# Performance work log

Measured on AMD Instinct MI355X. Metric: run time of the kernel, lower is better.

## Reference

```python
import jax, jax.numpy as jnp
import numpy as np

B, C, HH, WW = 2, 64, 56, 56
NH, IP, OP = 4, 32, 64  # num_heads, inter_plane, out_plane
EPS = 1e-5


def setup_inputs() -> dict:
    key = jax.random.key(0)
    ks = jax.random.split(key, 12)
    r = lambda k, sh, s: jax.random.normal(k, sh, jnp.float32) * s
    inp = {
        "x": r(ks[0], (B, C, HH, WW), 1.0),
        # 1x1 conv QKV projections: weight [out_ch, in_ch], kaiming-ish scale
        "wk": r(ks[1], (NH * IP, C), C ** -0.5), "bk": jnp.zeros((NH * IP,), jnp.float32),
        "wq": r(ks[2], (NH * IP, C), C ** -0.5), "bq": jnp.zeros((NH * IP,), jnp.float32),
        "wv": r(ks[3], (NH * IP, C), C ** -0.5), "bv": jnp.zeros((NH * IP,), jnp.float32),
        # GCN linears
        "w1": r(ks[4], (OP, IP), IP ** -0.5), "b1": jnp.zeros((OP,), jnp.float32),
        "g1": 1.0 + r(ks[5], (NH * OP,), 0.1), "be1": jnp.zeros((NH * OP,), jnp.float32),
        "rm1": jnp.zeros((NH * OP,), jnp.float32), "rv1": jnp.ones((NH * OP,), jnp.float32),
        "w2": r(ks[6], (OP, OP), OP ** -0.5), "b2": jnp.zeros((OP,), jnp.float32),
        "g2": 1.0 + r(ks[7], (NH * OP,), 0.1), "be2": jnp.zeros((NH * OP,), jnp.float32),
        "rm2": jnp.zeros((NH * OP,), jnp.float32), "rv2": jnp.ones((NH * OP,), jnp.float32),
        # final 1x1 projection
        "wf": r(ks[8], (OP, NH * OP), (NH * OP) ** -0.5), "bf": jnp.zeros((OP,), jnp.float32),
    }
    return inp


def _conv1x1(x, w, b):
    # x: [b,c,h,w], w: [o,c] -> [b,o,h,w]
    return jnp.einsum('bchw,oc->bohw', x, w) + b[None, :, None, None]


def _bn_relu(y, g, be, rm, rv, b, n):
    # y: [b,H,N,OP]; BatchNorm1d(H*OP) in eval mode over channel axis, then ReLU
    z = y.transpose(0, 1, 3, 2).reshape(b, NH * OP, n)  # [b, H*OP, N]
    z = (z - rm[None, :, None]) * (g / jnp.sqrt(rv + EPS))[None, :, None] + be[None, :, None]
    return jax.nn.relu(z.reshape(b, NH, OP, n).transpose(0, 1, 3, 2))  # [b,H,N,OP]


def reference(x, wk, bk, wq, bq, wv, bv, w1, b1, g1, be1, rm1, rv1,
              w2, b2, g2, be2, rm2, rv2, wf, bf):
    b, c, h, w = x.shape
    n = h * w
    node_k = _conv1x1(x, wk, bk).reshape(b, NH, IP, n).transpose(0, 1, 3, 2)  # [b,H,N,IP]
    node_q = _conv1x1(x, wq, bq).reshape(b, NH, IP, n)                        # [b,H,IP,N]
    node_v = _conv1x1(x, wv, bv).reshape(b, NH, IP, n).transpose(0, 1, 3, 2)  # [b,H,N,IP]
    adj = jnp.einsum('bhnd,bhdm->bhnm', node_k, node_q)  # [b,H,N,N]
    adj = jax.nn.softmax(adj, axis=2)  # NOTE: torch softmax(dim=2) -> normalize over rows axis
    av = jnp.einsum('bhnm,bhmd->bhnd', adj, node_v)      # [b,H,N,IP]
    avw = _bn_relu(av @ w1.T + b1, g1, be1, rm1, rv1, b, n)   # [b,H,N,OP]; dropout is identity (eval)
    av2 = jnp.einsum('bhnm,bhmd->bhnd', adj, avw)        # [b,H,N,OP]
    avw2 = _bn_relu(av2 @ w2.T + b2, g2, be2, rm2, rv2, b, n)  # [b,H,N,OP]
    y = avw2.transpose(0, 1, 3, 2).reshape(b, NH * OP, h, w)
    return _conv1x1(y, wf, bf)  # [b, OP, h, w]
```

## Files before the change

### kernel.cpp

```cpp
#include <hip/hip_runtime.h>
#include <hip/hip_bf16.h>

typedef __hip_bfloat16 bf16;
typedef __attribute__((ext_vector_type(8))) short bfrag;
typedef __attribute__((ext_vector_type(4))) short s16x4;
typedef __attribute__((ext_vector_type(4))) float f32x4;
typedef __attribute__((ext_vector_type(16))) float f32x16;

#define MFMA32(a,b,c) __builtin_amdgcn_mfma_f32_32x32x16_bf16((a),(b),(c),0,0,0)

__device__ __forceinline__ float b2f(bf16 x){ return __bfloat162float(x); }
__device__ __forceinline__ bf16 f2b(float x){ return __float2bfloat16(x); }
__device__ __forceinline__ float fexp2(float x){ return __builtin_amdgcn_exp2f(x); }
__device__ __forceinline__ float us2f(unsigned short u){ unsigned v = (unsigned)u << 16; return __uint_as_float(v); }

#define NN   3136
#define NBH  8
#define NCH  7
#define MCH  448
#define LDP  40
#define LDPA 72
#define LOG2E 1.44269504f

__global__ __launch_bounds__(256) void k_zero(float* __restrict__ p, int n4)
{
    int i = blockIdx.x * 256 + threadIdx.x;
    if (i < n4) reinterpret_cast<f32x4*>(p)[i] = (f32x4){0.f, 0.f, 0.f, 0.f};
}

__global__ __launch_bounds__(256) void k_proj(
    const float* __restrict__ x,
    const float* __restrict__ wk, const float* __restrict__ bk,
    const float* __restrict__ wq, const float* __restrict__ bq,
    const float* __restrict__ wv, const float* __restrict__ bv,
    bf16* __restrict__ kt, bf16* __restrict__ qt, bf16* __restrict__ vt)
{
    __shared__ __align__(16) bf16 xT[32 * 72];
    __shared__ __align__(16) bf16 wT[128 * 72];
    int tid = threadIdx.x, w = tid >> 6, lane = tid & 63;
    int l31 = lane & 31, lsel = lane >> 5;
    int n0 = blockIdx.x * 32;
    int p  = blockIdx.y;
    int b  = blockIdx.z;
    const float* wp = (p == 0) ? wk : ((p == 1) ? wq : wv);
    const float* bp = (p == 0) ? bk : ((p == 1) ? bq : bv);

    for (int i = tid; i < 2048; i += 256) {
        int c = i >> 5, j = i & 31;
        xT[j * 72 + c] = f2b(x[((size_t)b * 64 + c) * NN + n0 + j]);
    }
    for (int i = tid; i < 8192; i += 256) {
        int oc = i >> 6, c = i & 63;
        wT[oc * 72 + c] = f2b(wp[oc * 64 + c]);
    }
    __syncthreads();

    f32x16 s;
    #pragma unroll
    for (int r = 0; r < 16; ++r) s[r] = 0.f;
    #pragma unroll
    for (int k = 0; k < 4; ++k) {
        bfrag a  = *(const bfrag*)(&xT[l31 * 72 + k * 16 + lsel * 8]);
        bfrag bw = *(const bfrag*)(&wT[(w * 32 + l31) * 72 + k * 16 + lsel * 8]);
        s = MFMA32(a, bw, s);
    }
    float bias = bp[w * 32 + l31];
    size_t bh = (size_t)b * 4 + w;
    if (p == 2) {
        #pragma unroll
        for (int q = 0; q < 4; ++q) {
            s16x4 pk;
            #pragma unroll
            for (int i = 0; i < 4; ++i) {
                bf16 e = f2b(s[4 * q + i] + bias);
                pk[i] = *(short*)&e;
            }
            *(s16x4*)(vt + (bh * 32 + l31) * NN + n0 + 8 * q + 4 * lsel) = pk;
        }
    } else {
        bf16* dst = (p == 0) ? kt : qt;
        float sc = (p == 0) ? LOG2E : 1.0f;
        #pragma unroll
        for (int r = 0; r < 16; ++r) {
            int nl = (r & 3) + 8 * (r >> 2) + 4 * lsel;
            dst[(bh * NN + n0 + nl) * 32 + l31] = f2b((s[r] + bias) * sc);
        }
    }
}

__global__ __launch_bounds__(256) void k_stats(const bf16* __restrict__ kt,
                                               const bf16* __restrict__ qt,
                                               float* __restrict__ den)
{
    __shared__ __align__(16) bf16 Kb[2][64 * LDP];
    int tid = threadIdx.x, w = tid >> 6, lane = tid & 63;
    int l31 = lane & 31, lsel = lane >> 5;
    int bh = blockIdx.z;
    int mt = blockIdx.x * 4 + w;
    bool act = (mt < 98);
    int m0 = (act ? mt : 97) * 32;
    int ns = blockIdx.y * MCH;

    const bf16* qp = qt + ((size_t)bh * NN + m0 + l31) * 32 + lsel * 8;
    bfrag qb0 = *(const bfrag*)qp;
    bfrag qb1 = *(const bfrag*)(qp + 16);
    const bf16* kt_bh = kt + (size_t)bh * NN * 32;

    int sr = tid >> 2, sc = (tid & 3) * 8;
    const bf16* sbase = kt_bh + (size_t)(ns + sr) * 32 + sc;
    int soff = sr * LDP + sc;

    *(bfrag*)(&Kb[0][soff]) = *(const bfrag*)sbase;
    __syncthreads();

    float dacc = 0.f;
    for (int t = 0; t < 7; ++t) {
        bfrag pre;
        bool hn = (t + 1 < 7);
        if (hn) pre = *(const bfrag*)(sbase + (size_t)(t + 1) * 2048);
        const bf16* kl = &Kb[t & 1][0];
        #pragma unroll
        for (int nt = 0; nt < 2; ++nt) {
            int ko = (l31 + 32 * nt) * LDP + lsel * 8;
            bfrag kb0 = *(const bfrag*)(kl + ko);
            bfrag kb1 = *(const bfrag*)(kl + ko + 16);
            f32x16 s;
            #pragma unroll
            for (int r = 0; r < 16; ++r) s[r] = 0.f;
            s = MFMA32(kb0, qb0, s);
            s = MFMA32(kb1, qb1, s);
            float ps = 0.f;
            #pragma unroll
            for (int r = 0; r < 16; ++r) ps += fexp2(s[r]);
            dacc += ps;
        }
        if (hn) *(bfrag*)(&Kb[(t + 1) & 1][soff]) = pre;
        __syncthreads();
    }
    dacc += __shfl_xor(dacc, 32);
    if (act && lane < 32) atomicAdd(&den[(size_t)bh * NN + m0 + l31], dacc);
}

__global__ __launch_bounds__(256) void k_recip(float* __restrict__ den)
{
    int i = blockIdx.x * 256 + threadIdx.x;
    if (i < NBH * NN) den[i] = 1.0f / den[i];
}

__global__ __launch_bounds__(256) void k_scalev(bf16* __restrict__ vt, const float* __restrict__ rden)
{
    int by = blockIdx.y;
    const float* rdp = rden + ((size_t)(by >> 5)) * NN;
    bf16* vp = vt + (size_t)by * NN;
    int i = blockIdx.x * 256 + threadIdx.x;
    if (i < 392) {
        int m = i * 8;
        union { bfrag v; unsigned short us[8]; } u;
        u.v = *(const bfrag*)(vp + m);
        #pragma unroll
        for (int j = 0; j < 8; ++j) {
            bf16 e = f2b(us2f(u.us[j]) * rdp[m + j]);
            u.us[j] = *(unsigned short*)&e;
        }
        *(bfrag*)(vp + m) = u.v;
    }
}

__global__ __launch_bounds__(256) void k_av(const bf16* __restrict__ kt,
    const bf16* __restrict__ qt, const bf16* __restrict__ vtp,
    bf16* __restrict__ av_p)
{
    __shared__ __align__(16) bf16 Qb[2][64 * LDP];
    __shared__ __align__(16) bf16 Vb[2][32 * LDPA];
    int tid = threadIdx.x, w = tid >> 6, lane = tid & 63;
    int l31 = lane & 31, lsel = lane >> 5;
    int bh = blockIdx.z;
    int ntile = blockIdx.x * 4 + w;
    bool act = (ntile < 98);
    int n0 = (act ? ntile : 97) * 32;
    int ms = blockIdx.y * MCH;

    const bf16* kp = kt + ((size_t)bh * NN + n0 + l31) * 32 + lsel * 8;
    bfrag kb0 = *(const bfrag*)kp;
    bfrag kb1 = *(const bfrag*)(kp + 16);
    const bf16* qt_bh = qt + (size_t)bh * NN * 32;
    const bf16* vt_bh = vtp + (size_t)bh * 32 * NN;

    int qr = tid >> 2, qc = (tid & 3) * 8;
    const bf16* qsb = qt_bh + (size_t)(ms + qr) * 32 + qc;
    int qoff = qr * LDP + qc;
    int vr = tid >> 3, vc = (tid & 7) * 8;
    const bf16* vsb = vt_bh + (size_t)vr * NN + ms + vc;
    int voff = vr * LDPA + vc;

    *(bfrag*)(&Qb[0][qoff]) = *(const bfrag*)qsb;
    *(bfrag*)(&Vb[0][voff]) = *(const bfrag*)vsb;
    __syncthreads();

    f32x16 acc;
    #pragma unroll
    for (int r = 0; r < 16; ++r) acc[r] = 0.f;

    for (int t = 0; t < 7; ++t) {
        bfrag preQ, preV;
        bool hn = (t + 1 < 7);
        if (hn) {
            preQ = *(const bfrag*)(qsb + (size_t)(t + 1) * 2048);
            preV = *(const bfrag*)(vsb + (size_t)(t + 1) * 64);
        }
        const bf16* ql = &Qb[t & 1][0];
        const bf16* vl = &Vb[t & 1][0];
        #pragma unroll
        for (int mt2 = 0; mt2 < 2; ++mt2) {
            int qo = (l31 + 32 * mt2) * LDP + lsel * 8;
            bfrag q0 = *(const bfrag*)(ql + qo);
            bfrag q1 = *(const bfrag*)(ql + qo + 16);
            f32x16 s;
            #pragma unroll
            for (int r = 0; r < 16; ++r) s[r] = 0.f;
            s = MFMA32(q0, kb0, s);
            s = MFMA32(q1, kb1, s);
            union { unsigned short us[8]; bfrag v; } pa0, pa1;
            #pragma unroll
            for (int i = 0; i < 8; ++i) {
                bf16 e0 = f2b(fexp2(s[i]));
                bf16 e1 = f2b(fexp2(s[8 + i]));
                pa0.us[i] = *(unsigned short*)&e0;
                pa1.us[i] = *(unsigned short*)&e1;
            }
            const bf16* vrow = vl + l31 * LDPA + 32 * mt2 + lsel * 4;
            union { s16x4 h[2]; bfrag v; } vb0, vb1;
            vb0.h[0] = *(const s16x4*)(vrow);
            vb0.h[1] = *(const s16x4*)(vrow + 8);
            vb1.h[0] = *(const s16x4*)(vrow + 16);
            vb1.h[1] = *(const s16x4*)(vrow + 24);
            acc = MFMA32(pa0.v, vb0.v, acc);
            acc = MFMA32(pa1.v, vb1.v, acc);
        }
        if (hn) {
            *(bfrag*)(&Qb[(t + 1) & 1][qoff]) = preQ;
            *(bfrag*)(&Vb[(t + 1) & 1][voff]) = preV;
        }
        __syncthreads();
    }
    if (act) {
        bf16* dst = av_p + (size_t)blockIdx.y * ((size_t)NBH * NN * 32)
                  + ((size_t)bh * NN + n0) * 32 + l31;
        #pragma unroll
        for (int r = 0; r < 16; ++r) {
            int nl = (r & 3) + 8 * (r >> 2) + 4 * lsel;
            dst[(size_t)nl * 32] = f2b(acc[r]);
        }
    }
}

__global__ __launch_bounds__(256) void k_av2(const bf16* __restrict__ kt,
    const bf16* __restrict__ qt, const bf16* __restrict__ awts,
    bf16* __restrict__ av2_p)
{
    __shared__ __align__(16) bf16 Qb[2][64 * LDP];
    __shared__ __align__(16) bf16 Ab[2][64 * LDPA];
    int tid = threadIdx.x, w = tid >> 6, lane = tid & 63;
    int l31 = lane & 31, lsel = lane >> 5;
    int bh = blockIdx.z;
    int ntile = blockIdx.x * 4 + w;
    bool act = (ntile < 98);
    int n0 = (act ? ntile : 97) * 32;
    int ms = blockIdx.y * MCH;

    const bf16* kp = kt + ((size_t)bh * NN + n0 + l31) * 32 + lsel * 8;
    bfrag kb0 = *(const bfrag*)kp;
    bfrag kb1 = *(const bfrag*)(kp + 16);
    const bf16* qt_bh = qt + (size_t)bh * NN * 32;
    const bf16* aw_bh = awts + (size_t)bh * 64 * NN;

    int qr = tid >> 2, qc = (tid & 3) * 8;
    const bf16* qsb = qt_bh + (size_t)(ms + qr) * 32 + qc;
    int qoff = qr * LDP + qc;
    int ar0 = tid >> 3, acv = (tid & 7) * 8;
    const bf16* asb0 = aw_bh + (size_t)ar0 * NN + ms + acv;
    const bf16* asb1 = aw_bh + (size_t)(ar0 + 32) * NN + ms + acv;
    int aoff0 = ar0 * LDPA + acv;
    int aoff1 = (ar0 + 32) * LDPA + acv;

    *(bfrag*)(&Qb[0][qoff])  = *(const bfrag*)qsb;
    *(bfrag*)(&Ab[0][aoff0]) = *(const bfrag*)asb0;
    *(bfrag*)(&Ab[0][aoff1]) = *(const bfrag*)asb1;
    __syncthreads();

    f32x16 acc0, acc1;
    #pragma unroll
    for (int r = 0; r < 16; ++r) { acc0[r] = 0.f; acc1[r] = 0.f; }

    for (int t = 0; t < 7; ++t) {
        bfrag preQ, preA0, preA1;
        bool hn = (t + 1 < 7);
        if (hn) {
            preQ  = *(const bfrag*)(qsb  + (size_t)(t + 1) * 2048);
            preA0 = *(const bfrag*)(asb0 + (size_t)(t + 1) * 64);
            preA1 = *(const bfrag*)(asb1 + (size_t)(t + 1) * 64);
        }
        const bf16* ql = &Qb[t & 1][0];
        const bf16* al = &Ab[t & 1][0];
        #pragma unroll
        for (int mt2 = 0; mt2 < 2; ++mt2) {
            int qo = (l31 + 32 * mt2) * LDP + lsel * 8;
            bfrag q0 = *(const bfrag*)(ql + qo);
            bfrag q1 = *(const bfrag*)(ql + qo + 16);
            f32x16 s;
            #pragma unroll
            for (int r = 0; r < 16; ++r) s[r] = 0.f;
            s = MFMA32(q0, kb0, s);
            s = MFMA32(q1, kb1, s);
            union { unsigned short us[8]; bfrag v; } pa0, pa1;
            #pragma unroll
            for (int i = 0; i < 8; ++i) {
                bf16 e0 = f2b(fexp2(s[i]));
                bf16 e1 = f2b(fexp2(s[8 + i]));
                pa0.us[i] = *(unsigned short*)&e0;
                pa1.us[i] = *(unsigned short*)&e1;
            }
            const bf16* a0 = al + l31 * LDPA + 32 * mt2 + lsel * 4;
            const bf16* a1 = al + (l31 + 32) * LDPA + 32 * mt2 + lsel * 4;
            union { s16x4 h[2]; bfrag v; } e00, e01, e10, e11;
            e00.h[0] = *(const s16x4*)(a0);
            e00.h[1] = *(const s16x4*)(a0 + 8);
            e01.h[0] = *(const s16x4*)(a0 + 16);
            e01.h[1] = *(const s16x4*)(a0 + 24);
            e10.h[0] = *(const s16x4*)(a1);
            e10.h[1] = *(const s16x4*)(a1 + 8);
            e11.h[0] = *(const s16x4*)(a1 + 16);
            e11.h[1] = *(const s16x4*)(a1 + 24);
            acc0 = MFMA32(pa0.v, e00.v, acc0);
            acc0 = MFMA32(pa1.v, e01.v, acc0);
            acc1 = MFMA32(pa0.v, e10.v, acc1);
            acc1 = MFMA32(pa1.v, e11.v, acc1);
        }
        if (hn) {
            *(bfrag*)(&Qb[(t + 1) & 1][qoff])  = preQ;
            *(bfrag*)(&Ab[(t + 1) & 1][aoff0]) = preA0;
            *(bfrag*)(&Ab[(t + 1) & 1][aoff1]) = preA1;
        }
        __syncthreads();
    }
    if (act) {
        bf16* dst = av2_p + (size_t)blockIdx.y * ((size_t)NBH * NN * 64)
                  + ((size_t)bh * NN + n0) * 64 + l31;
        #pragma unroll
        for (int r = 0; r < 16; ++r) {
            int nl = (r & 3) + 8 * (r >> 2) + 4 * lsel;
            dst[(size_t)nl * 64]      = f2b(acc0[r]);
            dst[(size_t)nl * 64 + 32] = f2b(acc1[r]);
        }
    }
}

__global__ __launch_bounds__(256) void k_red1(const bf16* __restrict__ av_p,
    const float* __restrict__ w1, const float* __restrict__ b1,
    const float* __restrict__ g1, const float* __restrict__ be1,
    const float* __restrict__ rm1, const float* __restrict__ rv1,
    const float* __restrict__ rds,
    bf16* __restrict__ awts)
{
    __shared__ float avl[64 * 33];
    __shared__ float w1l[64 * 33];
    __shared__ float sc[64], sh[64], bb[64];
    int n0 = blockIdx.x * 64, bh = blockIdx.y, h = bh & 3;
    int tid = threadIdx.x;
    const size_t cstride = (size_t)NBH * NN * 32;
    const bf16* ap = av_p + ((size_t)bh * NN + n0) * 32;
    {
        int nr = tid >> 2, e8 = (tid & 3) * 8;
        int base = nr * 32 + e8;
        float s8[8];
        #pragma unroll
        for (int j = 0; j < 8; ++j) s8[j] = 0.f;
        #pragma unroll
        for (int c = 0; c < NCH; ++c) {
            union { bfrag v; unsigned short us[8]; } u;
            u.v = *(const bfrag*)(ap + (size_t)c * cstride + base);
            #pragma unroll
            for (int j = 0; j < 8; ++j) s8[j] += us2f(u.us[j]);
        }
        #pragma unroll
        for (int j = 0; j < 8; ++j) avl[nr * 33 + e8 + j] = s8[j];
    }
    for (int i = tid; i < 2048; i += 256)
        w1l[(i >> 5) * 33 + (i & 31)] = w1[i];
    if (tid < 64) {
        int ch = h * 64 + tid;
        float s = g1[ch] * rsqrtf(rv1[ch] + 1e-5f);
        sc[tid] = s; sh[tid] = be1[ch] - rm1[ch] * s; bb[tid] = b1[tid];
    }
    __syncthreads();
    int nb = (tid & 15) * 4, eb = (tid >> 4) * 4;
    float rsc[4];
    {
        const float* rp = rds + (size_t)bh * NN + n0 + nb;
        rsc[0] = rp[0]; rsc[1] = rp[1]; rsc[2] = rp[2]; rsc[3] = rp[3];
    }
    float s[4][4];
    #pragma unroll
    for (int i = 0; i < 4; ++i)
        #pragma unroll
        for (int j = 0; j < 4; ++j) s[i][j] = bb[eb + j];
    for (int d = 0; d < 32; ++d) {
        float a0 = avl[(nb+0)*33+d], a1 = avl[(nb+1)*33+d], a2 = avl[(nb+2)*33+d], a3 = avl[(nb+3)*33+d];
        float w0 = w1l[(eb+0)*33+d], w1v = w1l[(eb+1)*33+d], w2v = w1l[(eb+2)*33+d], w3 = w1l[(eb+3)*33+d];
        s[0][0]+=a0*w0; s[0][1]+=a0*w1v; s[0][2]+=a0*w2v; s[0][3]+=a0*w3;
        s[1][0]+=a1*w0; s[1][1]+=a1*w1v; s[1][2]+=a1*w2v; s[1][3]+=a1*w3;
        s[2][0]+=a2*w0; s[2][1]+=a2*w1v; s[2][2]+=a2*w2v; s[2][3]+=a2*w3;
        s[3][0]+=a3*w0; s[3][1]+=a3*w1v; s[3][2]+=a3*w2v; s[3][3]+=a3*w3;
    }
    #pragma unroll
    for (int j = 0; j < 4; ++j) {
        int e = eb + j;
        ushort4 pk;
        float v0 = fmaxf(s[0][j] * sc[e] + sh[e], 0.f) * rsc[0];
        float v1 = fmaxf(s[1][j] * sc[e] + sh[e], 0.f) * rsc[1];
        float v2 = fmaxf(s[2][j] * sc[e] + sh[e], 0.f) * rsc[2];
        float v3 = fmaxf(s[3][j] * sc[e] + sh[e], 0.f) * rsc[3];
        bf16 b0 = f2b(v0), b1b = f2b(v1), b2b = f2b(v2), b3 = f2b(v3);
        pk.x = *(unsigned short*)&b0; pk.y = *(unsigned short*)&b1b;
        pk.z = *(unsigned short*)&b2b; pk.w = *(unsigned short*)&b3;
        *reinterpret_cast<ushort4*>(awts + ((size_t)bh * 64 + e) * NN + n0 + nb) = pk;
    }
}

__global__ __launch_bounds__(256) void k_red2(const bf16* __restrict__ av2_p,
    const float* __restrict__ w2, const float* __restrict__ b2,
    const float* __restrict__ g2, const float* __restrict__ be2,
    const float* __restrict__ rm2, const float* __restrict__ rv2,
    bf16* __restrict__ y)
{
    __shared__ float a2l[64 * 65];
    __shared__ float w2l[64 * 65];
    __shared__ float sc[64], sh[64], bb[64];
    int n0 = blockIdx.x * 64, bh = blockIdx.y, h = bh & 3, b = bh >> 2;
    int tid = threadIdx.x;
    const size_t cstride = (size_t)NBH * NN * 64;
    const bf16* ap = av2_p + ((size_t)bh * NN + n0) * 64;
    #pragma unroll
    for (int it = 0; it < 2; ++it) {
        int idx = it * 256 + tid;
        int nr = idx >> 3, e8 = (idx & 7) * 8;
        int base = nr * 64 + e8;
        float s8[8];
        #pragma unroll
        for (int j = 0; j < 8; ++j) s8[j] = 0.f;
        #pragma unroll
        for (int c = 0; c < NCH; ++c) {
            union { bfrag v; unsigned short us[8]; } u;
            u.v = *(const bfrag*)(ap + (size_t)c * cstride + base);
            #pragma unroll
            for (int j = 0; j < 8; ++j) s8[j] += us2f(u.us[j]);
        }
        #pragma unroll
        for (int j = 0; j < 8; ++j) a2l[nr * 65 + e8 + j] = s8[j];
    }
    for (int i = tid; i < 4096; i += 256)
        w2l[(i >> 6) * 65 + (i & 63)] = w2[i];
    if (tid < 64) {
        int ch = h * 64 + tid;
        float s = g2[ch] * rsqrtf(rv2[ch] + 1e-5f);
        sc[tid] = s; sh[tid] = be2[ch] - rm2[ch] * s; bb[tid] = b2[tid];
    }
    __syncthreads();
    int nb = (tid & 15) * 4, eb = (tid >> 4) * 4;
    float s[4][4];
    #pragma unroll
    for (int i = 0; i < 4; ++i)
        #pragma unroll
        for (int j = 0; j < 4; ++j) s[i][j] = bb[eb + j];
    for (int d = 0; d < 64; ++d) {
        float a0 = a2l[(nb+0)*65+d], a1 = a2l[(nb+1)*65+d], a2 = a2l[(nb+2)*65+d], a3 = a2l[(nb+3)*65+d];
        float w0 = w2l[(eb+0)*65+d], w1v = w2l[(eb+1)*65+d], w2v = w2l[(eb+2)*65+d], w3 = w2l[(eb+3)*65+d];
        s[0][0]+=a0*w0; s[0][1]+=a0*w1v; s[0][2]+=a0*w2v; s[0][3]+=a0*w3;
        s[1][0]+=a1*w0; s[1][1]+=a1*w1v; s[1][2]+=a1*w2v; s[1][3]+=a1*w3;
        s[2][0]+=a2*w0; s[2][1]+=a2*w1v; s[2][2]+=a2*w2v; s[2][3]+=a2*w3;
        s[3][0]+=a3*w0; s[3][1]+=a3*w1v; s[3][2]+=a3*w2v; s[3][3]+=a3*w3;
    }
    #pragma unroll
    for (int j = 0; j < 4; ++j) {
        int e = eb + j;
        ushort4 pk;
        float v0 = fmaxf(s[0][j] * sc[e] + sh[e], 0.f);
        float v1 = fmaxf(s[1][j] * sc[e] + sh[e], 0.f);
        float v2 = fmaxf(s[2][j] * sc[e] + sh[e], 0.f);
        float v3 = fmaxf(s[3][j] * sc[e] + sh[e], 0.f);
        bf16 b0 = f2b(v0), b1b = f2b(v1), b2b = f2b(v2), b3 = f2b(v3);
        pk.x = *(unsigned short*)&b0; pk.y = *(unsigned short*)&b1b;
        pk.z = *(unsigned short*)&b2b; pk.w = *(unsigned short*)&b3;
        *reinterpret_cast<ushort4*>(y + ((size_t)b * 256 + h * 64 + e) * NN + n0 + nb) = pk;
    }
}

__global__ __launch_bounds__(256) void k_final(const bf16* __restrict__ y,
    const float* __restrict__ wf, const float* __restrict__ bf_,
    float* __restrict__ out)
{
    int t = blockIdx.x * 256 + threadIdx.x;
    int n = t * 2;
    if (n >= NN) return;
    int o = blockIdx.y;
    int b = blockIdx.z;
    float s0 = bf_[o], s1 = s0;
    const bf16* yp = y + (size_t)b * 256 * NN + n;
    const float* wp = wf + o * 256;
    #pragma unroll 16
    for (int k = 0; k < 256; ++k) {
        unsigned u = *reinterpret_cast<const unsigned*>(yp + (size_t)k * NN);
        float lo = __uint_as_float(u << 16);
        float hi = __uint_as_float(u & 0xffff0000u);
        s0 += wp[k] * lo;
        s1 += wp[k] * hi;
    }
    float* op = out + ((size_t)b * 64 + o) * NN + n;
    op[0] = s0;
    op[1] = s1;
}

extern "C" void kernel_launch(void* const* d_in, const int* in_sizes, int n_in,
                              void* d_out, int out_size, void* d_ws, size_t ws_size,
                              hipStream_t stream)
{
    const float* x   = (const float*)d_in[0];
    const float* wk  = (const float*)d_in[1];
    const float* bk  = (const float*)d_in[2];
    const float* wq  = (const float*)d_in[3];
    const float* bq  = (const float*)d_in[4];
    const float* wv  = (const float*)d_in[5];
    const float* bv  = (const float*)d_in[6];
    const float* w1  = (const float*)d_in[7];
    const float* b1  = (const float*)d_in[8];
    const float* g1  = (const float*)d_in[9];
    const float* be1 = (const float*)d_in[10];
    const float* rm1 = (const float*)d_in[11];
    const float* rv1 = (const float*)d_in[12];
    const float* w2  = (const float*)d_in[13];
    const float* b2  = (const float*)d_in[14];
    const float* g2  = (const float*)d_in[15];
    const float* be2 = (const float*)d_in[16];
    const float* rm2 = (const float*)d_in[17];
    const float* rv2 = (const float*)d_in[18];
    const float* wf  = (const float*)d_in[19];
    const float* bff = (const float*)d_in[20];
    float* out = (float*)d_out;

    char* ws = (char*)d_ws;
    bf16* kt   = (bf16*)ws;
    bf16* qt   = kt + (size_t)NBH * NN * 32;
    bf16* vt   = qt + (size_t)NBH * NN * 32;
    bf16* awts = vt + (size_t)NBH * 32 * NN;
    bf16* y    = awts + (size_t)NBH * 64 * NN;
    float* den = (float*)(y + (size_t)2 * 256 * NN);
    bf16* av_p  = (bf16*)(den + (size_t)NBH * NN);
    bf16* av2_p = av_p + (size_t)NCH * NBH * NN * 32;

    k_zero  <<<dim3(25),       256, 0, stream>>>(den, 6272);
    k_proj  <<<dim3(98, 3, 2), 256, 0, stream>>>(x, wk, bk, wq, bq, wv, bv, kt, qt, vt);
    k_stats <<<dim3(25, 7, 8), 256, 0, stream>>>(kt, qt, den);
    k_recip <<<dim3(98),       256, 0, stream>>>(den);
    k_scalev<<<dim3(2, 256),   256, 0, stream>>>(vt, den);
    k_av    <<<dim3(25, 7, 8), 256, 0, stream>>>(kt, qt, vt, av_p);
    k_red1  <<<dim3(49, 8),    256, 0, stream>>>(av_p, w1, b1, g1, be1, rm1, rv1, den, awts);
    k_av2   <<<dim3(25, 7, 8), 256, 0, stream>>>(kt, qt, awts, av2_p);
    k_red2  <<<dim3(49, 8),    256, 0, stream>>>(av2_p, w2, b2, g2, be2, rm2, rv2, y);
    k_final <<<dim3(7, 64, 2), 256, 0, stream>>>(y, wf, bff, out);
}
```

Baseline: 111.2 us.

## Transpose y layout and compute final projection with bf16 MFMA

k_red2 now writes y in node-major [b, N, 256] layout so each node's channels are contiguous. The scalar final 1x1 projection is replaced by a 32x32x16 bf16 MFMA kernel: four waves each cover a 64-channel slice of K and are summed through shared memory, with the weights converted to bf16 in LDS. This removes a long scalar FMA loop with strided global reads, at the cost of bf16 weight rounding and an LDS reduction step.

```diff
diff --git a/kernel.cpp b/kernel.cpp
--- a/kernel.cpp
+++ b/kernel.cpp
@@ -20,6 +20,7 @@
 #define MCH  448
 #define LDP  40
 #define LDPA 72
+#define LDW  272
 #define LOG2E 1.44269504f
 
 __global__ __launch_bounds__(256) void k_zero(float* __restrict__ p, int n4)
@@ -431,7 +432,7 @@
     const float* __restrict__ w2, const float* __restrict__ b2,
     const float* __restrict__ g2, const float* __restrict__ be2,
     const float* __restrict__ rm2, const float* __restrict__ rv2,
-    bf16* __restrict__ y)
+    bf16* __restrict__ yt)
 {
     __shared__ float a2l[64 * 65];
     __shared__ float w2l[64 * 65];
@@ -481,43 +482,61 @@
         s[3][0]+=a3*w0; s[3][1]+=a3*w1v; s[3][2]+=a3*w2v; s[3][3]+=a3*w3;
     }
     #pragma unroll
-    for (int j = 0; j < 4; ++j) {
-        int e = eb + j;
+    for (int i = 0; i < 4; ++i) {
         ushort4 pk;
-        float v0 = fmaxf(s[0][j] * sc[e] + sh[e], 0.f);
-        float v1 = fmaxf(s[1][j] * sc[e] + sh[e], 0.f);
-        float v2 = fmaxf(s[2][j] * sc[e] + sh[e], 0.f);
-        float v3 = fmaxf(s[3][j] * sc[e] + sh[e], 0.f);
+        float v0 = fmaxf(s[i][0] * sc[eb+0] + sh[eb+0], 0.f);
+        float v1 = fmaxf(s[i][1] * sc[eb+1] + sh[eb+1], 0.f);
+        float v2 = fmaxf(s[i][2] * sc[eb+2] + sh[eb+2], 0.f);
+        float v3 = fmaxf(s[i][3] * sc[eb+3] + sh[eb+3], 0.f);
         bf16 b0 = f2b(v0), b1b = f2b(v1), b2b = f2b(v2), b3 = f2b(v3);
         pk.x = *(unsigned short*)&b0; pk.y = *(unsigned short*)&b1b;
         pk.z = *(unsigned short*)&b2b; pk.w = *(unsigned short*)&b3;
-        *reinterpret_cast<ushort4*>(y + ((size_t)b * 256 + h * 64 + e) * NN + n0 + nb) = pk;
-    }
-}
-
-__global__ __launch_bounds__(256) void k_final(const bf16* __restrict__ y,
+        *reinterpret_cast<ushort4*>(yt + ((size_t)b * NN + n0 + nb + i) * 256 + h * 64 + eb) = pk;
+    }
+}
+
+__global__ __launch_bounds__(256) void k_finalM(const bf16* __restrict__ yt,
     const float* __restrict__ wf, const float* __restrict__ bf_,
     float* __restrict__ out)
 {
-    int t = blockIdx.x * 256 + threadIdx.x;
-    int n = t * 2;
-    if (n >= NN) return;
-    int o = blockIdx.y;
-    int b = blockIdx.z;
-    float s0 = bf_[o], s1 = s0;
-    const bf16* yp = y + (size_t)b * 256 * NN + n;
-    const float* wp = wf + o * 256;
-    #pragma unroll 16
-    for (int k = 0; k < 256; ++k) {
-        unsigned u = *reinterpret_cast<const unsigned*>(yp + (size_t)k * NN);
-        float lo = __uint_as_float(u << 16);
-        float hi = __uint_as_float(u & 0xffff0000u);
-        s0 += wp[k] * lo;
-        s1 += wp[k] * hi;
-    }
-    float* op = out + ((size_t)b * 64 + o) * NN + n;
-    op[0] = s0;
-    op[1] = s1;
+    __shared__ __align__(16) bf16 wfb[32 * LDW];
+    __shared__ float red[4 * 16 * 64];
+    int tid = threadIdx.x, w = tid >> 6, lane = tid & 63;
+    int l31 = lane & 31, lsel = lane >> 5;
+    int n0 = blockIdx.x * 32;
+    int b  = blockIdx.y;
+    int o0 = blockIdx.z * 32;
+
+    for (int i = tid; i < 8192; i += 256) {
+        int o = i >> 8, k = i & 255;
+        wfb[o * LDW + k] = f2b(wf[(size_t)(o0 + o) * 256 + k]);
+    }
+    __syncthreads();
+
+    const bf16* yb = yt + ((size_t)b * NN + n0 + l31) * 256 + w * 64 + lsel * 8;
+    const bf16* wb = &wfb[l31 * LDW + w * 64 + lsel * 8];
+    f32x16 s;
+    #pragma unroll
+    for (int r = 0; r < 16; ++r) s[r] = 0.f;
+    #pragma unroll
+    for (int kk = 0; kk < 4; ++kk) {
+        bfrag a  = *(const bfrag*)(wb + kk * 16);
+        bfrag bv = *(const bfrag*)(yb + kk * 16);
+        s = MFMA32(a, bv, s);
+    }
+    float* rp = &red[(w * 16) * 64 + lane];
+    #pragma unroll
+    for (int r = 0; r < 16; ++r) rp[r * 64] = s[r];
+    __syncthreads();
+
+    for (int idx = tid; idx < 1024; idx += 256) {
+        int ln = idx & 63, r = idx >> 6;
+        float v = red[r * 64 + ln] + red[(16 + r) * 64 + ln]
+                + red[(32 + r) * 64 + ln] + red[(48 + r) * 64 + ln];
+        int ol = (r & 3) + 8 * (r >> 2) + 4 * (ln >> 5);
+        int o = o0 + ol;
+        out[((size_t)b * 64 + o) * NN + n0 + (ln & 31)] = v + bf_[o];
+    }
 }
 
 extern "C" void kernel_launch(void* const* d_in, const int* in_sizes, int n_in,
@@ -552,8 +571,8 @@
     bf16* qt   = kt + (size_t)NBH * NN * 32;
     bf16* vt   = qt + (size_t)NBH * NN * 32;
     bf16* awts = vt + (size_t)NBH * 32 * NN;
-    bf16* y    = awts + (size_t)NBH * 64 * NN;
-    float* den = (float*)(y + (size_t)2 * 256 * NN);
+    bf16* yt   = awts + (size_t)NBH * 64 * NN;
+    float* den = (float*)(yt + (size_t)2 * NN * 256);
     bf16* av_p  = (bf16*)(den + (size_t)NBH * NN);
     bf16* av2_p = av_p + (size_t)NCH * NBH * NN * 32;
 
@@ -565,6 +584,6 @@
     k_av    <<<dim3(25, 7, 8), 256, 0, stream>>>(kt, qt, vt, av_p);
     k_red1  <<<dim3(49, 8),    256, 0, stream>>>(av_p, w1, b1, g1, be1, rm1, rv1, den, awts);
     k_av2   <<<dim3(25, 7, 8), 256, 0, stream>>>(kt, qt, awts, av2_p);
-    k_red2  <<<dim3(49, 8),    256, 0, stream>>>(av2_p, w2, b2, g2, be2, rm2, rv2, y);
-    k_final <<<dim3(7, 64, 2), 256, 0, stream>>>(y, wf, bff, out);
-}
+    k_red2  <<<dim3(49, 8),    256, 0, stream>>>(av2_p, w2, b2, g2, be2, rm2, rv2, yt);
+    k_finalM<<<dim3(98, 2, 2), 256, 0, stream>>>(yt, wf, bff, out);
+}
```

Result: faster. 103.9 us, median of 2 (-6.6%).
